# Performance work log

Hardware: AMD Instinct MI355X
Metric: run time of the kernel (lower is better)

## Reference

```python
import jax
import jax.numpy as jnp
import numpy as np
from jax import lax

DN = ('NCHW', 'OIHW', 'NCHW')


def _conv(x, w, b, stride, pad):
    y = lax.conv_general_dilated(x, w, (stride, stride), [(pad, pad), (pad, pad)],
                                 dimension_numbers=DN)
    return y + b[None, :, None, None]


def _conv_t(x, w, b, stride, pad):
    # torch ConvTranspose2d(w shape: (Cin, Cout, kh, kw)) == fractionally-strided conv
    # with spatially-flipped, IO-swapped kernel and padding k-1-p.
    k = w.shape[2]
    wf = jnp.transpose(jnp.flip(w, (2, 3)), (1, 0, 2, 3))  # (Cout, Cin, kh, kw)
    q = k - 1 - pad
    y = lax.conv_general_dilated(x, wf, (1, 1), [(q, q), (q, q)],
                                 lhs_dilation=(stride, stride), dimension_numbers=DN)
    return y + b[None, :, None, None]


def setup_inputs() -> dict:
    key = jax.random.key(0)
    ks = jax.random.split(key, 16)
    K, D = 512, 256  # codebook_size, codebook_len
    s = lambda k, shp, fan: jax.random.normal(k, shp, jnp.float32) * (1.0 / np.sqrt(fan))
    return {
        'x': jax.random.normal(ks[0], (16, 3, 256, 256), jnp.float32),
        'w_enc1': s(ks[1], (D // 4, 3, 4, 4), 3 * 16),
        'b_enc1': jnp.zeros((D // 4,), jnp.float32),
        'w_enc2': s(ks[2], (D // 2, D // 4, 4, 4), (D // 4) * 16),
        'b_enc2': jnp.zeros((D // 2,), jnp.float32),
        'w_prevq': s(ks[3], (D, D // 2, 3, 3), (D // 2) * 9),
        'b_prevq': jnp.zeros((D,), jnp.float32),
        'emb': jax.random.uniform(ks[4], (K, D), jnp.float32, -1.0 / K, 1.0 / K),
        'w_post': s(ks[5], (D, D // 2, 4, 4), D * 16),   # ConvTranspose2d(in,out,...)
        'b_post': jnp.zeros((D // 2,), jnp.float32),
        'w_dec1': s(ks[6], (D // 2, D // 4, 4, 4), (D // 2) * 16),
        'b_dec1': jnp.zeros((D // 4,), jnp.float32),
        'w_dec2': s(ks[7], (D // 4, 3, 3, 3), (D // 4) * 9),
        'b_dec2': jnp.zeros((3,), jnp.float32),
    }


def reference(x, w_enc1, b_enc1, w_enc2, b_enc2, w_prevq, b_prevq, emb,
              w_post, b_post, w_dec1, b_dec1, w_dec2, b_dec2):
    # --- Encoder ---
    h = jax.nn.relu(_conv(x, w_enc1, b_enc1, 2, 1))
    h = jax.nn.relu(_conv(h, w_enc2, b_enc2, 2, 1))
    z = _conv(h, w_prevq, b_prevq, 1, 1)          # (B, D, H/4, W/4)

    # --- VQ (NHWC layout) ---
    z_e = jnp.transpose(z, (0, 2, 3, 1))           # (B, h, w, D)
    D = z_e.shape[-1]
    K = emb.shape[0]
    flat = z_e.reshape(-1, D)                      # (N, D)
    dist = (jnp.sum(flat * flat, axis=1, keepdims=True)
            + jnp.sum(emb * emb, axis=1)
            - 2.0 * flat @ emb.T)                  # (N, K)
    idx = jnp.argmin(dist, axis=1)                 # (N,)
    enc = jax.nn.one_hot(idx, K, dtype=flat.dtype) # (N, K) one-hot scatter
    z_q = (enc @ emb).reshape(z_e.shape)           # dense gather-matmul (faithful)
    avg_probs = jnp.mean(enc, axis=0)
    perplexity = jnp.exp(-jnp.sum(avg_probs * jnp.log(avg_probs + 1e-10)))

    # straight-through estimator, back to NCHW
    dec_in = jnp.transpose(z_e + lax.stop_gradient(z_q - z_e), (0, 3, 1, 2))

    # --- Decoder ---
    d = _conv_t(dec_in, w_post, b_post, 2, 1)      # no ReLU after post_vq
    d = jax.nn.relu(_conv_t(d, w_dec1, b_dec1, 2, 1))
    x_recon = _conv_t(d, w_dec2, b_dec2, 1, 1)
    return (x_recon, z_e, z_q, perplexity)
```

## Files before the change

### kernel.cpp

```cpp
#include <hip/hip_runtime.h>
#include <stdint.h>


typedef unsigned short bfraw;
typedef __attribute__((ext_vector_type(8))) short s16x8;
typedef __attribute__((ext_vector_type(4))) float f32x4;

__device__ __forceinline__ float bflo(unsigned int u) {
    union { unsigned int i; float f; } v; v.i = u << 16; return v.f;
}
__device__ __forceinline__ float bfhi(unsigned int u) {
    union { unsigned int i; float f; } v; v.i = u & 0xFFFF0000u; return v.f;
}
__device__ __forceinline__ bfraw f2bf(float f) {
    union { float f; unsigned int i; } v; v.f = f;
    unsigned int r = v.i + 0x7FFFu + ((v.i >> 16) & 1u);
    return (bfraw)(r >> 16);
}

__device__ __forceinline__ void gl_lds16(const void* g, void* l) {
    auto gp = reinterpret_cast<const __attribute__((address_space(1))) unsigned int*>(
        reinterpret_cast<uintptr_t>(g));
    auto lp = reinterpret_cast<__attribute__((address_space(3))) unsigned int*>(
        reinterpret_cast<uintptr_t>(l));
    __builtin_amdgcn_global_load_lds(gp, lp, 16, 0, 0);
}

__global__ void wtb_kernel(const float* __restrict__ w, bfraw* __restrict__ wt,
                           int Cout, int Cin, int KH, int KW, int transposed) {
    int n = Cout * Cin * KH * KW;
    int NT = KH * KW;
    for (int i = blockIdx.x * blockDim.x + threadIdx.x; i < n; i += gridDim.x * blockDim.x) {
        int ci = i % Cin; int t = i / Cin;
        int tap = t % NT; int co = t / NT;
        int kh = tap / KW, kw = tap % KW;
        float v = transposed ? w[(((long)ci * Cout + co) * KH + kh) * KW + kw]
                             : w[(((long)co * Cin + ci) * KH + kh) * KW + kw];
        wt[i] = f2bf(v);
    }
}

__global__ void wb2_kernel(const float* __restrict__ w, bfraw* __restrict__ wt) {
    int i = blockIdx.x * 256 + threadIdx.x;
    if (i >= 9216) return;
    int ci = i & 63; int t = i >> 6;
    int tap = t % 9, co = t / 9;
    bfraw v = 0;
    if (co < 3) {
        int kh = 2 - tap / 3, kw = 2 - tap % 3;
        v = f2bf(w[(((long)ci * 3 + co) * 3 + kh) * 3 + kw]);
    }
    wt[(long)co * 576 + tap * 64 + ci] = v;
}

__global__ void wb1_kernel(const float* __restrict__ w, bfraw* __restrict__ wt) {
    int i = blockIdx.x * 256 + threadIdx.x;
    if (i >= 4096) return;
    int k = i & 63, co = i >> 6;
    bfraw v = 0;
    if (k < 48) {
        int ci = k % 3, tap = k / 3, kh = tap >> 2, kw = tap & 3;
        v = f2bf(w[(((long)co * 3 + ci) * 4 + kh) * 4 + kw]);
    }
    wt[(long)co * 64 + k] = v;
}

__global__ __launch_bounds__(256) void xpack_kernel(const float* __restrict__ x,
                                                    bfraw* __restrict__ a0) {
    int pos = blockIdx.x * 256 + threadIdx.x;
    int ow = pos & 127, oh = (pos >> 7) & 127, n = pos >> 14;
    __align__(16) bfraw v[64];
#pragma unroll
    for (int i = 0; i < 64; ++i) v[i] = 0;
#pragma unroll
    for (int kh = 0; kh < 4; ++kh) {
        int ih = 2 * oh - 1 + kh; if ((unsigned)ih >= 256u) continue;
#pragma unroll
        for (int kw = 0; kw < 4; ++kw) {
            int iw = 2 * ow - 1 + kw; if ((unsigned)iw >= 256u) continue;
#pragma unroll
            for (int ci = 0; ci < 3; ++ci)
                v[(kh * 4 + kw) * 3 + ci] =
                    f2bf(x[(((long)n * 3 + ci) * 256 + ih) * 256 + iw]);
        }
    }
    uint4* dst = (uint4*)(a0 + (long)pos * 64);
    const uint4* src = (const uint4*)v;
#pragma unroll
    for (int i = 0; i < 8; ++i) dst[i] = src[i];
}

__global__ void embsq_kernel(const float* __restrict__ emb, float* __restrict__ esq) {
    int k = blockIdx.x, lane = threadIdx.x;
    float s = 0.f;
    for (int d = lane; d < 256; d += 64) { float v = emb[k * 256 + d]; s += v * v; }
    for (int o = 32; o; o >>= 1) s += __shfl_down(s, o, 64);
    if (lane == 0) esq[k] = s;
}

template<int BM, int BN, int WM, int WN, bool TR, bool RELU, bool OUTF32, bool DUALB>
__global__ __launch_bounds__(256) void igemm_kernel(
    const bfraw* __restrict__ in, const bfraw* __restrict__ wt,
    const float* __restrict__ bias, void* __restrict__ outv,
    bfraw* __restrict__ outb, const bfraw* __restrict__ zp,
    int Hin, int Win, int Cin, int sf, int NTW, int Ksteps,
    int lw, int lh, int N, int KW, int pad,
    unsigned long long pk0, unsigned long long pk1,
    unsigned long long pk2, unsigned long long pk3)
{
    constexpr int APASS = BM / 64, BPASS = BN / 64;
    __shared__ __align__(16) bfraw ldsA[2][BM * 32];
    __shared__ __align__(16) bfraw ldsB[2][BN * 32];
    const int tid = threadIdx.x, lane = tid & 63, wv = tid >> 6;
    const int wm = wv / WN, wn = wv % WN;
    const int lrow = lane >> 2, lkof = (lane & 3) * 8;
    const int n0 = blockIdx.y * BN;
    const int Wm1 = (1 << lw) - 1, Hm1 = (1 << lh) - 1;
    const int bid = blockIdx.x;
    int blockM, cls;
    if (TR) {
        cls = (bid >> 3) & 3;
        blockM = (bid & 7) * ((int)gridDim.x >> 5) + (bid >> 5);
    } else {
        cls = 0;
        blockM = (bid & 7) * ((int)gridDim.x >> 3) + (bid >> 3);
    }
    const unsigned long long pack = (cls == 0) ? pk0 : (cls == 1) ? pk1
                                  : (cls == 2) ? pk2 : pk3;
    const int py = cls >> 1, px = cls & 1;

    long baseA[APASS]; int ihb[APASS], iwb[APASS];
#pragma unroll
    for (int p = 0; p < APASS; ++p) {
        int m = p * 64 + wv * 16 + lrow;
        int pos = blockM * BM + m;
        int ow = pos & Wm1; int t = pos >> lw;
        int oh = t & Hm1;   int nb = t >> lh;
        ihb[p] = oh * sf; iwb[p] = ow * sf;
        baseA[p] = ((long)(nb * Hin + ihb[p]) * Win + iwb[p]) * (long)Cin + lkof;
    }
    long baseB[BPASS];
#pragma unroll
    for (int p = 0; p < BPASS; ++p) {
        int nl = p * 64 + wv * 16 + lrow;
        baseB[p] = (long)(n0 + nl) * ((long)NTW * Cin) + lkof;
    }

    f32x4 acc[4][4];
#pragma unroll
    for (int i = 0; i < 4; ++i)
#pragma unroll
        for (int j = 0; j < 4; ++j) acc[i][j] = (f32x4)0.f;

    int ci0 = 0, tslot = 0, dy, dx, wk;
    if (TR) {
        unsigned e = (unsigned)pack & 0xFFFFu;
        dy = (int)((e >> 8) & 3) - 1; dx = (int)((e >> 4) & 3) - 1; wk = (int)(e & 15u);
    } else { dy = -pad; dx = -pad; wk = 0; }

    const int quad = lane >> 4, r16 = lane & 15;

    auto stage = [&](int buf) {
        long offA = ((long)(dy * Win + dx)) * Cin + ci0;
        long offB = (long)wk * Cin + ci0;
#pragma unroll
        for (int p = 0; p < APASS; ++p) {
            int ih = ihb[p] + dy, iw = iwb[p] + dx;
            bool ok = ((unsigned)ih < (unsigned)Hin) & ((unsigned)iw < (unsigned)Win);
            const bfraw* g = ok ? (in + baseA[p] + offA) : (zp + lkof);
            gl_lds16(g, &ldsA[buf][(p * 64 + wv * 16) * 32]);
        }
#pragma unroll
        for (int p = 0; p < BPASS; ++p)
            gl_lds16(wt + baseB[p] + offB, &ldsB[buf][(p * 64 + wv * 16) * 32]);
    };
    auto advance = [&]() {
        ci0 += 32;
        if (ci0 == Cin) {
            ci0 = 0; ++tslot;
            if (TR) {
                unsigned e = (unsigned)(pack >> ((tslot & 3) * 16)) & 0xFFFFu;
                dy = (int)((e >> 8) & 3) - 1; dx = (int)((e >> 4) & 3) - 1; wk = (int)(e & 15u);
            } else { ++wk; ++dx; if (dx == KW - pad) { dx = -pad; ++dy; } }
        }
    };

    stage(0); advance();
    __syncthreads();

    for (int ks = 0; ks < Ksteps; ++ks) {
        const int cur = ks & 1;
        if (ks + 1 < Ksteps) { stage(cur ^ 1); advance(); }
        s16x8 af[4], bf[4];
#pragma unroll
        for (int i = 0; i < 4; ++i)
            af[i] = *(const s16x8*)&ldsA[cur][(wm * 64 + i * 16 + r16) * 32 + quad * 8];
#pragma unroll
        for (int j = 0; j < 4; ++j)
            bf[j] = *(const s16x8*)&ldsB[cur][(wn * 64 + j * 16 + r16) * 32 + quad * 8];
#pragma unroll
        for (int i = 0; i < 4; ++i)
#pragma unroll
            for (int j = 0; j < 4; ++j)
                acc[i][j] = __builtin_amdgcn_mfma_f32_16x16x32_bf16(af[i], bf[j], acc[i][j], 0, 0, 0);
        __syncthreads();
    }

#pragma unroll
    for (int j = 0; j < 4; ++j) {
        int col = wn * 64 + j * 16 + r16; int ng = n0 + col;
        float bv = bias[ng];
#pragma unroll
        for (int i = 0; i < 4; ++i) {
            int mb = wm * 64 + i * 16 + quad * 4;
#pragma unroll
            for (int r = 0; r < 4; ++r) {
                int pos2 = blockM * BM + mb + r;
                long oaddr;
                if (TR) {
                    int ow2 = pos2 & Wm1; int t = pos2 >> lw;
                    int oh2 = t & Hm1;    int nb = t >> lh;
                    int oh = 2 * oh2 + py, ow = 2 * ow2 + px;
                    oaddr = ((long)(((nb << (lh + 1)) + oh) << (lw + 1)) + ow) * N + ng;
                } else {
                    oaddr = (long)pos2 * N + ng;
                }
                float v = acc[i][j][r] + bv;
                if (RELU) v = fmaxf(v, 0.f);
                if (OUTF32) {
                    ((float*)outv)[oaddr] = v;
                    if (DUALB) outb[oaddr] = f2bf(v);
                } else {
                    ((bfraw*)outv)[oaddr] = f2bf(v);
                }
            }
        }
    }
}

__global__ __launch_bounds__(256) void dec2m_kernel(
    const bfraw* __restrict__ in, const bfraw* __restrict__ wb2,
    const float* __restrict__ bias, float* __restrict__ out,
    const bfraw* __restrict__ zp) {
    __shared__ __align__(16) bfraw tile[18 * 18 * 64];
    __shared__ __align__(16) bfraw ldsB[16 * 576];
    const int tid = threadIdx.x;
    const int b = blockIdx.x;
    const int n = b >> 8, t8 = b & 255;
    const int r0 = (t8 >> 4) * 16, c0 = (t8 & 15) * 16;
    const int wv = tid >> 6, lane = tid & 63;
    const int quad = lane >> 4, r16 = lane & 15;
    const long nbase = (long)n * 65536;

#pragma unroll
    for (int k = 0; k < 10; ++k) {
        int t = k * 256 + tid;
        int px = t >> 3, d = t & 7;
        int pr = px / 18, pc = px - pr * 18;
        int ih = r0 - 1 + pr, iw = c0 - 1 + pc;
        bool ok = ((unsigned)ih < 256u) & ((unsigned)iw < 256u);
        int s = d ^ (px & 7);
        const bfraw* g = ok ? in + ((nbase + (long)ih * 256 + iw) << 6) + s * 8 : zp;
        gl_lds16(g, &tile[(k * 256 + wv * 64) * 8]);
    }
    if (tid < 32) {
        int t = 2560 + tid;
        int px = t >> 3, d = t & 7;
        int pr = px / 18, pc = px - pr * 18;
        int ih = r0 - 1 + pr, iw = c0 - 1 + pc;
        bool ok = ((unsigned)ih < 256u) & ((unsigned)iw < 256u);
        int s = d ^ (px & 7);
        const bfraw* g = ok ? in + ((nbase + (long)ih * 256 + iw) << 6) + s * 8 : zp;
        gl_lds16(g, &tile[2560 * 8]);
    }
#pragma unroll
    for (int k = 0; k < 4; ++k) {
        int t = k * 256 + tid;
        int c = t / 72, s = t - c * 72;
        gl_lds16(wb2 + (long)c * 576 + ((s ^ (c & 7)) << 3), &ldsB[(k * 256 + wv * 64) * 8]);
    }
    if (tid < 128) {
        int t = 1024 + tid;
        int c = t / 72, s = t - c * 72;
        gl_lds16(wb2 + (long)c * 576 + ((s ^ (c & 7)) << 3), &ldsB[(1024 + wv * 64) * 8]);
    }
    __syncthreads();

    f32x4 acc[4];
#pragma unroll
    for (int i = 0; i < 4; ++i) acc[i] = (f32x4)0.f;

    int qb[4];
#pragma unroll
    for (int i = 0; i < 4; ++i) qb[i] = (wv * 4 + i + 1) * 18 + (r16 + 1);

#pragma unroll
    for (int ks = 0; ks < 18; ++ks) {
        const int tap = ks >> 1, h = ks & 1;
        const int dy = tap / 3 - 1, dx = tap % 3 - 1;
        s16x8 bfr = *(const s16x8*)&ldsB[r16 * 576 + (((ks * 4 + quad) ^ (r16 & 7)) << 3)];
        s16x8 afr[4];
#pragma unroll
        for (int i = 0; i < 4; ++i) {
            int q = qb[i] + dy * 18 + dx;
            afr[i] = *(const s16x8*)&tile[(q << 6) + ((((h << 2) + quad) ^ (q & 7)) << 3)];
        }
#pragma unroll
        for (int i = 0; i < 4; ++i)
            acc[i] = __builtin_amdgcn_mfma_f32_16x16x32_bf16(afr[i], bfr, acc[i], 0, 0, 0);
    }

    if (r16 < 3) {
        float bv = bias[r16];
        float* plane = out + (((long)(n * 3 + r16)) << 16);
#pragma unroll
        for (int i = 0; i < 4; ++i) {
            int oh = r0 + wv * 4 + i;
#pragma unroll
            for (int r = 0; r < 4; ++r) {
                int ow = c0 + quad * 4 + r;
                plane[((long)oh << 8) + ow] = acc[i][r] + bv;
            }
        }
    }
}

__global__ __launch_bounds__(256) void vqm_kernel(
    const bfraw* __restrict__ zeb, const bfraw* __restrict__ embB,
    const float* __restrict__ esq, float2* __restrict__ pb)
{
    __shared__ __align__(16) bfraw ldsA[128 * 32];
    __shared__ __align__(16) bfraw ldsB[128 * 32];
    __shared__ float sEsq[128];
    __shared__ float sVal[2][128];
    __shared__ int   sKey[2][128];
    const int tid = threadIdx.x, lane = tid & 63, wv = tid >> 6;
    const int wm = wv >> 1, wn = wv & 1;
    const int lrow = lane >> 2, lkof = (lane & 3) * 8;
    const int quad = lane >> 4, r16 = lane & 15;
    const int posBase = blockIdx.x * 128;
    const int codeBase = blockIdx.y * 128;

    if (tid < 128) sEsq[tid] = esq[codeBase + tid];

    const long baseA0 = (long)(posBase + wv * 16 + lrow) * 256 + lkof;
    const long baseA1 = baseA0 + 64 * 256;
    const long baseB0 = (long)(codeBase + wv * 16 + lrow) * 256 + lkof;
    const long baseB1 = baseB0 + 64 * 256;

    f32x4 acc[4][4];
#pragma unroll
    for (int i = 0; i < 4; ++i)
#pragma unroll
        for (int j = 0; j < 4; ++j) acc[i][j] = (f32x4)0.f;

    for (int k = 0; k < 8; ++k) {
        gl_lds16(zeb + baseA0 + k * 32, &ldsA[(wv * 16) * 32]);
        gl_lds16(zeb + baseA1 + k * 32, &ldsA[(64 + wv * 16) * 32]);
        gl_lds16(embB + baseB0 + k * 32, &ldsB[(wv * 16) * 32]);
        gl_lds16(embB + baseB1 + k * 32, &ldsB[(64 + wv * 16) * 32]);
        __syncthreads();
        s16x8 af[4], bf[4];
#pragma unroll
        for (int i = 0; i < 4; ++i)
            af[i] = *(const s16x8*)&ldsA[(wm * 64 + i * 16 + r16) * 32 + quad * 8];
#pragma unroll
        for (int j = 0; j < 4; ++j)
            bf[j] = *(const s16x8*)&ldsB[(wn * 64 + j * 16 + r16) * 32 + quad * 8];
#pragma unroll
        for (int i = 0; i < 4; ++i)
#pragma unroll
            for (int j = 0; j < 4; ++j)
                acc[i][j] = __builtin_amdgcn_mfma_f32_16x16x32_bf16(af[i], bf[j], acc[i][j], 0, 0, 0);
        __syncthreads();
    }

#pragma unroll
    for (int i = 0; i < 4; ++i) {
#pragma unroll
        for (int r = 0; r < 4; ++r) {
            float v = 1e30f; int kk = 1 << 30;
#pragma unroll
            for (int j = 0; j < 4; ++j) {
                int code = codeBase + wn * 64 + j * 16 + r16;
                float d = sEsq[wn * 64 + j * 16 + r16] - 2.f * acc[i][j][r];
                if (d < v) { v = d; kk = code; }
            }
#pragma unroll
            for (int m = 1; m < 16; m <<= 1) {
                float ov = __shfl_xor(v, m, 64);
                int   ok = __shfl_xor(kk, m, 64);
                if (ov < v || (ov == v && ok < kk)) { v = ov; kk = ok; }
            }
            if (r16 == 0) {
                int localRow = wm * 64 + i * 16 + quad * 4 + r;
                sVal[wn][localRow] = v;
                sKey[wn][localRow] = kk;
            }
        }
    }
    __syncthreads();
    if (tid < 128) {
        float v0 = sVal[0][tid]; int k0 = sKey[0][tid];
        float v1 = sVal[1][tid]; int k1 = sKey[1][tid];
        bool take1 = (v1 < v0) || (v1 == v0 && k1 < k0);
        float2 p; p.x = take1 ? v1 : v0;
        p.y = __int_as_float(take1 ? k1 : k0);
        pb[(long)blockIdx.y * 65536 + posBase + tid] = p;
    }
}

__global__ __launch_bounds__(256) void vqg_kernel(
    const float2* __restrict__ pb, const float* __restrict__ emb,
    float* __restrict__ zq, bfraw* __restrict__ zqb, int* __restrict__ hist)
{
    __shared__ int sIdxL[32];
    const int tid = threadIdx.x;
    const int posBase = blockIdx.x * 32;
    if (tid < 32) {
        float bv = 1e30f; int bk = 1 << 30;
#pragma unroll
        for (int c = 0; c < 4; ++c) {
            float2 p = pb[(long)c * 65536 + posBase + tid];
            int k = __float_as_int(p.y);
            if (p.x < bv || (p.x == bv && k < bk)) { bv = p.x; bk = k; }
        }
        sIdxL[tid] = bk;
        atomicAdd(&hist[bk], 1);
    }
    __syncthreads();
    const float4* emb4 = (const float4*)emb;
    float4*  zq4  = (float4*)(zq + (long)posBase * 256);
    ushort4* zqb4 = (ushort4*)(zqb + (long)posBase * 256);
#pragma unroll
    for (int it = 0; it < 8; ++it) {
        int i2 = it * 256 + tid;
        int p = i2 >> 6, c = i2 & 63;
        float4 vv = emb4[(long)sIdxL[p] * 64 + c];
        zq4[i2] = vv;
        ushort4 u; u.x = f2bf(vv.x); u.y = f2bf(vv.y); u.z = f2bf(vv.z); u.w = f2bf(vv.w);
        zqb4[i2] = u;
    }
}

__global__ void ppl_kernel(const int* __restrict__ hist, float* __restrict__ outp) {
    __shared__ float red[512];
    int t = threadIdx.x;
    float p = (float)hist[t] * (1.0f / 65536.0f);
    red[t] = p * logf(p + 1e-10f);
    __syncthreads();
    for (int s = 256; s; s >>= 1) { if (t < s) red[t] += red[t + s]; __syncthreads(); }
    if (t == 0) *outp = expf(-red[0]);
}

static unsigned long long packFor(int py, int px) {
    unsigned long long pk = 0; int s = 0;
    for (int kh = 0; kh < 4; ++kh) {
        if (((py + 1 - kh) & 1) != 0) continue;
        int dy = (py + 1 - kh) / 2;
        for (int kw = 0; kw < 4; ++kw) {
            if (((px + 1 - kw) & 1) != 0) continue;
            int dx = (px + 1 - kw) / 2;
            unsigned e = ((unsigned)(dy + 1) << 8) | ((unsigned)(dx + 1) << 4) | (unsigned)(kh * 4 + kw);
            pk |= (unsigned long long)e << (16 * s); ++s;
        }
    }
    return pk;
}

extern "C" void kernel_launch(void* const* d_in, const int* in_sizes, int n_in,
                              void* d_out, int out_size, void* d_ws, size_t ws_size,
                              hipStream_t stream) {
    const float* x       = (const float*)d_in[0];
    const float* w_enc1  = (const float*)d_in[1];
    const float* b_enc1  = (const float*)d_in[2];
    const float* w_enc2  = (const float*)d_in[3];
    const float* b_enc2  = (const float*)d_in[4];
    const float* w_prevq = (const float*)d_in[5];
    const float* b_prevq = (const float*)d_in[6];
    const float* emb     = (const float*)d_in[7];
    const float* w_post  = (const float*)d_in[8];
    const float* b_post  = (const float*)d_in[9];
    const float* w_dec1  = (const float*)d_in[10];
    const float* b_dec1  = (const float*)d_in[11];
    const float* w_dec2  = (const float*)d_in[12];
    const float* b_dec2  = (const float*)d_in[13];

    float* out = (float*)d_out;
    float* xr  = out;
    float* ze  = out + 3145728;
    float* zq  = ze + 16777216;
    float* ppl = zq + 16777216;

    char* W = (char*)d_ws;
    float* esq  = (float*)(W + 24576);
    int*   hist = (int*)(W + 28672);
    bfraw* zp   = (bfraw*)(W + 32768);
    bfraw* wb2  = (bfraw*)(W + 262144);
    bfraw* w2b  = (bfraw*)(W + 560128);
    bfraw* w3b  = (bfraw*)(W + 822272);
    bfraw* wpb  = (bfraw*)(W + 1412096);
    bfraw* wd1b = (bfraw*)(W + 2460672);
    bfraw* wb1  = (bfraw*)(W + 2722816);
    bfraw* embB = (bfraw*)(W + 2736128);
    char* bufX = W + 4194304;
    bfraw* a0    = (bfraw*)bufX;
    bfraw* h2    = (bfraw*)bufX;
    bfraw* zeb   = (bfraw*)(bufX + 16777216);
    bfraw* zqb   = (bfraw*)(bufX + 50331648);
    bfraw* ddec1 = (bfraw*)bufX;
    float2* pb   = (float2*)bufX;
    bfraw* dpost = (bfraw*)(W + 138412032);
    bfraw* h1    = (bfraw*)ze;

    wb2_kernel<<<36, 256, 0, stream>>>(w_dec2, wb2);
    wb1_kernel<<<16, 256, 0, stream>>>(w_enc1, wb1);
    wtb_kernel<<<512, 256, 0, stream>>>(w_enc2, w2b, 128, 64, 4, 4, 0);
    wtb_kernel<<<1152, 256, 0, stream>>>(w_prevq, w3b, 256, 128, 3, 3, 0);
    wtb_kernel<<<2048, 256, 0, stream>>>(w_post, wpb, 128, 256, 4, 4, 1);
    wtb_kernel<<<512, 256, 0, stream>>>(w_dec1, wd1b, 64, 128, 4, 4, 1);
    wtb_kernel<<<512, 256, 0, stream>>>(emb, embB, 512, 256, 1, 1, 0);
    embsq_kernel<<<512, 64, 0, stream>>>(emb, esq);
    hipMemsetAsync(hist, 0, 512 * sizeof(int), stream);
    hipMemsetAsync(zp, 0, 256, stream);

    xpack_kernel<<<1024, 256, 0, stream>>>(x, a0);
    igemm_kernel<256, 64, 4, 1, false, true, false, false><<<dim3(1024, 1, 1), 256, 0, stream>>>(
        a0, wb1, b_enc1, h1, nullptr, zp, 512, 512, 64, 1, 1, 2, 9, 9, 64, 1, 0,
        0ULL, 0ULL, 0ULL, 0ULL);
    igemm_kernel<128, 128, 2, 2, false, true, false, false><<<dim3(512, 1, 1), 256, 0, stream>>>(
        h1, w2b, b_enc2, h2, nullptr, zp, 128, 128, 64, 2, 16, 32, 6, 6, 128, 4, 1,
        0ULL, 0ULL, 0ULL, 0ULL);
    igemm_kernel<128, 128, 2, 2, false, false, true, true><<<dim3(512, 2, 1), 256, 0, stream>>>(
        h2, w3b, b_prevq, ze, zeb, zp, 64, 64, 128, 1, 9, 36, 6, 6, 256, 3, 1,
        0ULL, 0ULL, 0ULL, 0ULL);

    vqm_kernel<<<dim3(512, 4), 256, 0, stream>>>(zeb, embB, esq, pb);
    vqg_kernel<<<2048, 256, 0, stream>>>(pb, emb, zq, zqb, hist);
    ppl_kernel<<<1, 512, 0, stream>>>(hist, ppl);

    igemm_kernel<128, 128, 2, 2, true, false, false, false><<<dim3(2048, 1, 1), 256, 0, stream>>>(
        zqb, wpb, b_post, dpost, nullptr, zp, 64, 64, 256, 1, 16, 32, 6, 6, 128, 4, 1,
        packFor(0, 0), packFor(0, 1), packFor(1, 0), packFor(1, 1));
    igemm_kernel<256, 64, 4, 1, true, true, false, false><<<dim3(4096, 1, 1), 256, 0, stream>>>(
        dpost, wd1b, b_dec1, ddec1, nullptr, zp, 128, 128, 128, 1, 16, 16, 7, 7, 64, 4, 1,
        packFor(0, 0), packFor(0, 1), packFor(1, 0), packFor(1, 1));
    dec2m_kernel<<<4096, 256, 0, stream>>>(ddec1, wb2, b_dec2, xr, zp);
}
```

Before: 701.7 us.

## Swizzle LDS k-chunk slots in igemm and precompute per-tap staging pointers

Each lane's global source column chunk is XOR-swizzled by its row index, so the gl_lds16 writes land data in a permuted slot layout. The MFMA fragment reads use the matching swizzled slot, which is meant to cut LDS bank conflicts on the 16-byte fragment loads. Staging addresses are now computed once per filter tap in a retap helper and then bumped by 32 elements per channel step, which removes per-step address arithmetic and bounds checks. The zero-pad buffer memset grows to cover the swizzled offsets. The risk is that the swizzle and the read pattern fall out of sync and corrupt results, and that holding the pointers adds register pressure.

```diff
diff --git a/kernel.cpp b/kernel.cpp
--- a/kernel.cpp
+++ b/kernel.cpp
@@ -113,7 +113,8 @@
     __shared__ __align__(16) bfraw ldsB[2][BN * 32];
     const int tid = threadIdx.x, lane = tid & 63, wv = tid >> 6;
     const int wm = wv / WN, wn = wv % WN;
-    const int lrow = lane >> 2, lkof = (lane & 3) * 8;
+    const int lrow = lane >> 2;
+    const int lkofs = (((lane & 3) ^ (lrow & 3))) * 8;
     const int n0 = blockIdx.y * BN;
     const int Wm1 = (1 << lw) - 1, Hm1 = (1 << lh) - 1;
     const int bid = blockIdx.x;
@@ -137,13 +138,13 @@
         int ow = pos & Wm1; int t = pos >> lw;
         int oh = t & Hm1;   int nb = t >> lh;
         ihb[p] = oh * sf; iwb[p] = ow * sf;
-        baseA[p] = ((long)(nb * Hin + ihb[p]) * Win + iwb[p]) * (long)Cin + lkof;
+        baseA[p] = ((long)(nb * Hin + ihb[p]) * Win + iwb[p]) * (long)Cin + lkofs;
     }
     long baseB[BPASS];
 #pragma unroll
     for (int p = 0; p < BPASS; ++p) {
         int nl = p * 64 + wv * 16 + lrow;
-        baseB[p] = (long)(n0 + nl) * ((long)NTW * Cin) + lkof;
+        baseB[p] = (long)(n0 + nl) * ((long)NTW * Cin) + lkofs;
     }
 
     f32x4 acc[4][4];
@@ -159,20 +160,31 @@
     } else { dy = -pad; dx = -pad; wk = 0; }
 
     const int quad = lane >> 4, r16 = lane & 15;
-
-    auto stage = [&](int buf) {
-        long offA = ((long)(dy * Win + dx)) * Cin + ci0;
-        long offB = (long)wk * Cin + ci0;
+    const int rslot = ((quad ^ (r16 & 3)) << 3);
+
+    const bfraw* pA[APASS];
+    const bfraw* pB[BPASS];
+
+    auto retap = [&]() {
+        long offA = ((long)(dy * Win + dx)) * Cin;
 #pragma unroll
         for (int p = 0; p < APASS; ++p) {
             int ih = ihb[p] + dy, iw = iwb[p] + dx;
             bool ok = ((unsigned)ih < (unsigned)Hin) & ((unsigned)iw < (unsigned)Win);
-            const bfraw* g = ok ? (in + baseA[p] + offA) : (zp + lkof);
-            gl_lds16(g, &ldsA[buf][(p * 64 + wv * 16) * 32]);
-        }
+            pA[p] = ok ? (in + baseA[p] + offA) : (zp + lkofs);
+        }
+        long offB = (long)wk * Cin;
 #pragma unroll
         for (int p = 0; p < BPASS; ++p)
-            gl_lds16(wt + baseB[p] + offB, &ldsB[buf][(p * 64 + wv * 16) * 32]);
+            pB[p] = wt + baseB[p] + offB;
+    };
+    auto stage = [&](int buf) {
+#pragma unroll
+        for (int p = 0; p < APASS; ++p)
+            gl_lds16(pA[p], &ldsA[buf][(p * 64 + wv * 16) * 32]);
+#pragma unroll
+        for (int p = 0; p < BPASS; ++p)
+            gl_lds16(pB[p], &ldsB[buf][(p * 64 + wv * 16) * 32]);
     };
     auto advance = [&]() {
         ci0 += 32;
@@ -182,9 +194,16 @@
                 unsigned e = (unsigned)(pack >> ((tslot & 3) * 16)) & 0xFFFFu;
                 dy = (int)((e >> 8) & 3) - 1; dx = (int)((e >> 4) & 3) - 1; wk = (int)(e & 15u);
             } else { ++wk; ++dx; if (dx == KW - pad) { dx = -pad; ++dy; } }
+            retap();
+        } else {
+#pragma unroll
+            for (int p = 0; p < APASS; ++p) pA[p] += 32;
+#pragma unroll
+            for (int p = 0; p < BPASS; ++p) pB[p] += 32;
         }
     };
 
+    retap();
     stage(0); advance();
     __syncthreads();
 
@@ -194,10 +213,10 @@
         s16x8 af[4], bf[4];
 #pragma unroll
         for (int i = 0; i < 4; ++i)
-            af[i] = *(const s16x8*)&ldsA[cur][(wm * 64 + i * 16 + r16) * 32 + quad * 8];
+            af[i] = *(const s16x8*)&ldsA[cur][(wm * 64 + i * 16 + r16) * 32 + rslot];
 #pragma unroll
         for (int j = 0; j < 4; ++j)
-            bf[j] = *(const s16x8*)&ldsB[cur][(wn * 64 + j * 16 + r16) * 32 + quad * 8];
+            bf[j] = *(const s16x8*)&ldsB[cur][(wn * 64 + j * 16 + r16) * 32 + rslot];
 #pragma unroll
         for (int i = 0; i < 4; ++i)
 #pragma unroll
@@ -522,7 +541,7 @@
     wtb_kernel<<<512, 256, 0, stream>>>(emb, embB, 512, 256, 1, 1, 0);
     embsq_kernel<<<512, 64, 0, stream>>>(emb, esq);
     hipMemsetAsync(hist, 0, 512 * sizeof(int), stream);
-    hipMemsetAsync(zp, 0, 256, stream);
+    hipMemsetAsync(zp, 0, 1024, stream);
 
     xpack_kernel<<<1024, 256, 0, stream>>>(x, a0);
     igemm_kernel<256, 64, 4, 1, false, true, false, false><<<dim3(1024, 1, 1), 256, 0, stream>>>(
```

Result: no change. 697.0 us (-0.7%).
